# Performance work log

Measured on AMD Instinct MI355X. Metric: run time of the kernel, lower is better.

Reference implementation:

```python
import jax, jax.numpy as jnp
import numpy as np

B, T, C = 2, 2048, 2048
NH, NKV, HD = 16, 8, 256
SOFTCAP = 50.0
ROPE_BASE = 10000.0


def setup_inputs() -> dict:
    key = jax.random.key(0)
    ks = jax.random.split(key, 5)
    s = 0.02
    return {
        "X": jax.random.normal(ks[0], (B, T, C), dtype=jnp.float32),
        "Wq": jax.random.normal(ks[1], (C, NH * HD), dtype=jnp.float32) * s,
        "Wk": jax.random.normal(ks[2], (C, NKV * HD), dtype=jnp.float32) * s,
        "Wv": jax.random.normal(ks[3], (C, NKV * HD), dtype=jnp.float32) * s,
        "Wo": jax.random.normal(ks[4], (NH * HD, C), dtype=jnp.float32) * s,
    }


def _rotate_half(x):
    x1, x2 = x[..., : x.shape[-1] // 2], x[..., x.shape[-1] // 2 :]
    return jnp.concatenate((-x2, x1), axis=-1)


def _rope_cos_sin(t, head_dim, dtype):
    inv_freq = 1.0 / ROPE_BASE ** (
        jnp.arange(0, head_dim, 2, dtype=jnp.int32).astype(jnp.float32) / head_dim
    )  # [HD/2]
    pos = jnp.arange(t, dtype=jnp.float32)  # [T]
    freqs = pos[:, None] * inv_freq[None, :]  # [T, HD/2]
    emb = jnp.concatenate((freqs, freqs), axis=-1)  # [T, HD]
    # shape [1, 1, T, HD] to broadcast over (B, H, T, HD)
    return (
        jnp.cos(emb).astype(dtype)[None, None],
        jnp.sin(emb).astype(dtype)[None, None],
    )


def reference(X, Wq, Wk, Wv, Wo):
    b, t, c = X.shape
    n_rep = NH // NKV

    q = (X @ Wq).reshape(b, t, NH, HD).transpose(0, 2, 1, 3)   # [B,NH,T,HD]
    k = (X @ Wk).reshape(b, t, NKV, HD).transpose(0, 2, 1, 3)  # [B,NKV,T,HD]
    v = (X @ Wv).reshape(b, t, NKV, HD).transpose(0, 2, 1, 3)

    cos, sin = _rope_cos_sin(t, HD, X.dtype)
    q = q * cos + _rotate_half(q) * sin
    k = k * cos + _rotate_half(k) * sin

    # repeat_kv (GQA): [B,NKV,T,HD] -> [B,NH,T,HD]
    k = jnp.repeat(k, n_rep, axis=1)
    v = jnp.repeat(v, n_rep, axis=1)

    scale = 256.0 ** (-0.5)  # hardcoded in source
    att = jnp.einsum("bhqd,bhkd->bhqk", q, k) * scale
    # tanh logit softcapping
    att = SOFTCAP * jnp.tanh(att / SOFTCAP)
    # causal mask
    causal = jnp.tril(jnp.ones((t, t), dtype=bool))
    att = jnp.where(causal[None, None], att, -jnp.inf)
    att = jax.nn.softmax(att, axis=-1)

    y = jnp.einsum("bhqk,bhkd->bhqd", att, v)  # [B,NH,T,HD]
    y = y.transpose(0, 2, 1, 3).reshape(b, t, NH * HD)
    return y @ Wo
```

## Files before the change

### kernel.cpp

```cpp
#include <hip/hip_runtime.h>
#include <hip/hip_bf16.h>

#define NHD 16
#define NKVH 8
#define HDIM 256
#define TSEQ 2048
#define BATCH 2

typedef unsigned int   u32;
typedef unsigned short u16;

typedef __attribute__((ext_vector_type(8))) short bf16x8;
typedef __attribute__((ext_vector_type(4))) float floatx4;

__device__ inline u32 cvt2bf(float lo, float hi) {
  u32 r;
  asm("v_cvt_pk_bf16_f32 %0, %1, %2" : "=v"(r) : "v"(lo), "v"(hi));
  return r;
}
__device__ inline u16 f2bf(float f) {
  union { float f; u32 i; } v; v.f = f;
  u32 r = v.i + 0x7fffu + ((v.i >> 16) & 1u);
  return (u16)(r >> 16);
}
__device__ inline float bf2f(u16 u) {
  union { u32 i; float f; } v; v.i = ((u32)u) << 16; return v.f;
}
__device__ inline float fexp2(float x) {
  float r; asm("v_exp_f32 %0, %1" : "=v"(r) : "v"(x)); return r;
}
__device__ inline float fsin(float x) {
  float r; asm("v_sin_f32 %0, %1" : "=v"(r) : "v"(x)); return r;
}
__device__ inline float fcos(float x) {
  float r; asm("v_cos_f32 %0, %1" : "=v"(r) : "v"(x)); return r;
}
__device__ inline float ffract(float x) {
  float r; asm("v_fract_f32 %0, %1" : "=v"(r) : "v"(x)); return r;
}

typedef const __attribute__((address_space(1))) u32* gptr_t;
typedef __attribute__((address_space(3))) u32* lptr_t;
__device__ inline void gl_lds16(const void* g, void* l) {
  __builtin_amdgcn_global_load_lds((gptr_t)g, (lptr_t)l, 16, 0, 0);
}

__device__ inline void tconv_body(const float* __restrict__ in,
                                  u16* __restrict__ out, int R, int Cc,
                                  int bx, int by, int tid) {
  __shared__ float tile[64][65];
  const int r0 = by * 64, c0 = bx * 64;
  const int tr = tid >> 4;
  const int tc = (tid & 15) * 4;
#pragma unroll
  for (int j = 0; j < 4; ++j) {
    float4 v = *(const float4*)(in + (size_t)(r0 + tr + j * 16) * Cc + c0 + tc);
    tile[tr + j * 16][tc + 0] = v.x;
    tile[tr + j * 16][tc + 1] = v.y;
    tile[tr + j * 16][tc + 2] = v.z;
    tile[tr + j * 16][tc + 3] = v.w;
  }
  __syncthreads();
#pragma unroll
  for (int j = 0; j < 4; ++j) {
    int c = tr + j * 16;
    u16 o[4];
#pragma unroll
    for (int i = 0; i < 4; ++i) o[i] = f2bf(tile[tc + i][c]);
    *(uint2*)(out + (size_t)(c0 + c) * R + r0 + tc) = *(const uint2*)o;
  }
}

__global__ __launch_bounds__(256) void tconv_k(
    const float* __restrict__ in, u16* __restrict__ out, int R, int Cc)
{
  tconv_body(in, out, R, Cc, blockIdx.x, blockIdx.y, threadIdx.x);
}

__global__ __launch_bounds__(256) void xconv_k(
    const float* __restrict__ in, u16* __restrict__ out)
{
  size_t i = (size_t)blockIdx.x * 256 + threadIdx.x;
  float4 a = *(const float4*)(in + i * 8);
  float4 b = *(const float4*)(in + i * 8 + 4);
  uint4 o;
  o.x = cvt2bf(a.x, a.y); o.y = cvt2bf(a.z, a.w);
  o.z = cvt2bf(b.x, b.y); o.w = cvt2bf(b.z, b.w);
  *(uint4*)(out + i * 8) = o;
}

__global__ __launch_bounds__(256) void prep_k(
    const float* __restrict__ X,  const float* __restrict__ Wq,
    const float* __restrict__ Wk, const float* __restrict__ Wv,
    u16* __restrict__ XB, u16* __restrict__ WqT, u16* __restrict__ WkvT)
{
  const int bid = blockIdx.x, tid = threadIdx.x;
  if (bid < 4096) {
    size_t i = (size_t)bid * 256 + tid;
    float4 a = *(const float4*)(X + i * 8);
    float4 b = *(const float4*)(X + i * 8 + 4);
    uint4 o;
    o.x = cvt2bf(a.x, a.y); o.y = cvt2bf(a.z, a.w);
    o.z = cvt2bf(b.x, b.y); o.w = cvt2bf(b.z, b.w);
    *(uint4*)(XB + i * 8) = o;
  } else if (bid < 6144) {
    int idx = bid - 4096;
    tconv_body(Wq, WqT, 2048, 4096, idx & 63, idx >> 6, tid);
  } else if (bid < 7168) {
    int idx = bid - 6144;
    tconv_body(Wk, WkvT, 2048, 2048, idx & 31, idx >> 5, tid);
  } else {
    int idx = bid - 7168;
    tconv_body(Wv, WkvT + (size_t)2048 * 2048, 2048, 2048, idx & 31, idx >> 5, tid);
  }
}

template<int EPI, int BM>
__global__ __launch_bounds__(512, 2) void gemm256_k(
    const u16* __restrict__ Ab, const u16* __restrict__ BTp,
    void* __restrict__ Op, int M, int N, int K)
{
  constexpr int NI = BM / 32;
  constexpr int AI = BM / 64;
  __shared__ u16 LA[2][BM * 64];
  __shared__ u16 LB[2][256 * 64];
  const int t = threadIdx.x;
  const int lane = t & 63, wave = t >> 6;
  const int lg = lane >> 4, l15 = lane & 15;
  const int wm = wave >> 2, wn = wave & 3;
  const int mtiles = M / BM;
  const int mt = (int)blockIdx.x % mtiles, nt = (int)blockIdx.x / mtiles;
  const int m0 = mt * BM, n0 = nt << 8;

  const int arow = wave * (BM / 8) + (lane >> 3);
  const int ska  = ((lane & 7) ^ (arow & 7)) << 3;
  const int brow = wave * 32 + (lane >> 3);
  const int skb  = ((lane & 7) ^ (brow & 7)) << 3;
  const u16* Ag = Ab  + (size_t)(m0 + arow) * K + ska;
  const u16* Bg = BTp + (size_t)(n0 + brow) * K + skb;

  auto STAGE = [&](int k0, int sel) {
#pragma unroll
    for (int q = 0; q < AI; ++q)
      gl_lds16(Ag + k0 + (size_t)q * 8 * K, &LA[sel][(wave * (BM / 8) + q * 8) * 64]);
#pragma unroll
    for (int q = 0; q < 4; ++q)
      gl_lds16(Bg + k0 + (size_t)q * 8 * K, &LB[sel][(wave * 32 + q * 8) * 64]);
  };

  floatx4 acc[NI][4];
#pragma unroll
  for (int i = 0; i < NI; ++i)
#pragma unroll
    for (int j = 0; j < 4; ++j) acc[i][j] = (floatx4){0.f, 0.f, 0.f, 0.f};

  STAGE(0, 0);
  const int KT = K >> 6;
  for (int kt = 0; kt < KT; ++kt) {
    const int sel = kt & 1;
    if (kt + 1 < KT) {
      STAGE((kt + 1) << 6, sel ^ 1);
      if constexpr (BM == 256) asm volatile("s_waitcnt vmcnt(8)" ::: "memory");
      else                     asm volatile("s_waitcnt vmcnt(6)" ::: "memory");
    } else {
      asm volatile("s_waitcnt vmcnt(0)" ::: "memory");
    }
    __builtin_amdgcn_s_barrier();
    __builtin_amdgcn_sched_barrier(0);
    __builtin_amdgcn_s_setprio(1);
#pragma unroll
    for (int ks = 0; ks < 2; ++ks) {
      const int c = (ks << 2) + lg;
      bf16x8 bfv[4];
#pragma unroll
      for (int j = 0; j < 4; ++j) {
        int row = (EPI == 0) ? (wn * 64 + (j << 4) + l15)
                             : (wn * 32 + ((j & 1) << 4) + ((j >> 1) << 7) + l15);
        bfv[j] = *(const bf16x8*)(&LB[sel][row * 64 + ((c ^ (row & 7)) << 3)]);
      }
#pragma unroll
      for (int i = 0; i < NI; ++i) {
        int row = wm * (BM / 2) + (i << 4) + l15;
        bf16x8 af = *(const bf16x8*)(&LA[sel][row * 64 + ((c ^ (row & 7)) << 3)]);
#pragma unroll
        for (int j = 0; j < 4; ++j)
          acc[i][j] = __builtin_amdgcn_mfma_f32_16x16x32_bf16(af, bfv[j], acc[i][j], 0, 0, 0);
      }
    }
    __builtin_amdgcn_s_setprio(0);
    __builtin_amdgcn_s_barrier();
  }

  if constexpr (EPI == 0) {
#pragma unroll
    for (int i = 0; i < NI; ++i)
#pragma unroll
      for (int j = 0; j < 4; ++j)
#pragma unroll
        for (int r = 0; r < 4; ++r) {
          int m = m0 + wm * (BM / 2) + (i << 4) + (lg << 2) + r;
          int n = n0 + wn * 64 + (j << 4) + l15;
          ((float*)Op)[(size_t)m * N + n] = acc[i][j][r];
        }
  } else {
    float invf2[2];
#pragma unroll
    for (int j = 0; j < 2; ++j) {
      int col = wn * 32 + (j << 4) + l15;
      invf2[j] = fexp2(fmaf(-(float)col, 0.103810253f, -2.651496129f));
    }
#pragma unroll
    for (int i = 0; i < NI; ++i) {
#pragma unroll
      for (int j = 0; j < 2; ++j) {
        int col = wn * 32 + (j << 4) + l15;
        int n_lo = n0 + col;
#pragma unroll
        for (int r = 0; r < 4; ++r) {
          int m = m0 + wm * (BM / 2) + (i << 4) + (lg << 2) + r;
          int bb = m >> 11, tt = m & 2047;
          float vlo = acc[i][j][r], vhi = acc[i][j + 2][r];
          if (EPI == 1 || n_lo < 2048) {
            float rev = ffract((float)tt * invf2[j]);
            float sn = fsin(rev), cs = fcos(rev);
            float olo = vlo * cs - vhi * sn;
            float ohi = vhi * cs + vlo * sn;
            vlo = olo; vhi = ohi;
          }
          if (EPI == 1) {
            int h = n_lo >> 8;
            u16* dst = (u16*)Op + (((size_t)bb * NHD + h) * TSEQ + tt) * HDIM + col;
            dst[0]   = f2bf(vlo);
            dst[128] = f2bf(vhi);
          } else {
            if (n_lo < 2048) {
              int h = n_lo >> 8;
              u16* dst = (u16*)Op + (((size_t)bb * NKVH + h) * TSEQ + tt) * HDIM + col;
              dst[0]   = f2bf(vlo);
              dst[128] = f2bf(vhi);
            } else {
              int n2 = n_lo - 2048;
              int h = n2 >> 8;
              u16* dst = (u16*)Op + 8388608u +
                         (((size_t)bb * NKVH + h) * HDIM + col) * TSEQ + tt;
              dst[0] = f2bf(vlo);
              dst[(size_t)128 * TSEQ] = f2bf(vhi);
            }
          }
        }
      }
    }
  }
}

__global__ __launch_bounds__(512, 2) void attn_k(
    const u16* __restrict__ Q, const u16* __restrict__ Kb,
    const u16* __restrict__ Vt, u16* __restrict__ Y)
{
  __shared__ u16 Ks2[2][32 * 256];
  __shared__ u16 Vs[256 * 32];
  __shared__ u16 Ps[8 * 16 * 32];
  __shared__ float Ls[8][16];
  const int t = threadIdx.x, lane = t & 63, w = t >> 6;
  const int lg = lane >> 4, l15 = lane & 15;
  const int hq = w >> 2, wq = w & 3;
  const int qt = 31 - (int)blockIdx.y;
  const int hkv = (int)blockIdx.x >> 1, b = (int)blockIdx.x & 1;
  const int h = 2 * hkv + hq;

  const u16* Kg = Kb + ((size_t)(b * NKVH + hkv)) * TSEQ * HDIM;
  const u16* Vg = Vt + ((size_t)(b * NKVH + hkv)) * HDIM * TSEQ;

  int koff[2], voff[2];
#pragma unroll
  for (int q = 0; q < 2; ++q) {
    int krow = w * 4 + q * 2 + (lane >> 5);
    int kcc  = lane & 31;
    koff[q] = krow * 256 + ((kcc ^ (krow & 7)) << 3);
    int vd  = w * 32 + q * 16 + (lane >> 2);
    voff[q] = vd * TSEQ + (((lane & 3) ^ ((vd >> 2) & 3)) << 3);
  }

  auto STAGE_K = [&](int st, int sel) {
    const u16* kbase = Kg + (size_t)st * (32 * 256);
#pragma unroll
    for (int q = 0; q < 2; ++q)
      gl_lds16(kbase + koff[q], &Ks2[sel][(w * 4 + q * 2) * 256]);
  };
  auto STAGE_V = [&](int st) {
    const u16* vbase = Vg + st * 32;
#pragma unroll
    for (int q = 0; q < 2; ++q)
      gl_lds16(vbase + voff[q], &Vs[(w * 32 + q * 16) * 32]);
  };

  const u16* Qg = Q + (((size_t)(b * NHD + h)) * TSEQ + qt * 64 + wq * 16 + l15) * HDIM;
  bf16x8 qf[8];
#pragma unroll
  for (int ks = 0; ks < 8; ++ks) qf[ks] = *(const bf16x8*)(Qg + ks * 32 + lg * 8);

  floatx4 accY[16];
#pragma unroll
  for (int i = 0; i < 16; ++i) accY[i] = (floatx4){0.f, 0.f, 0.f, 0.f};
  float rsum = 0.f;

  const int qglob = qt * 64 + wq * 16 + l15;
  const int qmaxw = qt * 64 + wq * 16 + 15;
  const int nst = 2 * qt + 2;
  const int fps = (l15 ^ (l15 >> 2)) & 3;

  STAGE_K(0, 0);
  for (int st = 0; st < nst; ++st) {
    const int sel = st & 1;
    STAGE_V(st);
    if (st + 1 < nst) {
      STAGE_K(st + 1, sel ^ 1);
      asm volatile("s_waitcnt vmcnt(4)" ::: "memory");
    } else {
      asm volatile("s_waitcnt vmcnt(2)" ::: "memory");
    }
    __builtin_amdgcn_s_barrier();
    __builtin_amdgcn_sched_barrier(0);

    if (st * 32 <= qmaxw) {
      __builtin_amdgcn_s_setprio(1);
#pragma unroll
      for (int stile = 0; stile < 2; ++stile) {
        floatx4 sa0 = (floatx4){0.f, 0.f, 0.f, 0.f};
        floatx4 sa1 = (floatx4){0.f, 0.f, 0.f, 0.f};
#pragma unroll
        for (int ks = 0; ks < 8; ++ks) {
          int row = (stile << 4) + l15;
          int c = (ks << 2) + lg;
          bf16x8 kf = *(const bf16x8*)((const char*)Ks2[sel] +
                        row * 512 + ((c ^ (row & 7)) << 4));
          if (ks & 1)
            sa1 = __builtin_amdgcn_mfma_f32_16x16x32_bf16(kf, qf[ks], sa1, 0, 0, 0);
          else
            sa0 = __builtin_amdgcn_mfma_f32_16x16x32_bf16(kf, qf[ks], sa0, 0, 0, 0);
        }
        int sbase = st * 32 + (stile << 4) + (lg << 2);
        float p[4];
#pragma unroll
        for (int r = 0; r < 4; ++r) {
          float s = sa0[r] + sa1[r];
          float tt = fmaf(s * s, -5.2083333e-7f, 1.0f);
          float pv = fexp2(s * 0.0901684403f * tt);
          pv = (sbase + r <= qglob) ? pv : 0.0f;
          p[r] = pv;
          rsum += pv;
        }
        uint2 pw;
        pw.x = cvt2bf(p[0], p[1]);
        pw.y = cvt2bf(p[2], p[3]);
        int o = (stile << 5) + (lg << 3);
        int gran = (o >> 4) ^ fps;
        *(uint2*)((char*)Ps + (w << 10) + l15 * 64 + (gran << 4) + (o & 15)) = pw;
      }
      __builtin_amdgcn_s_setprio(0);
    }

    if (st + 1 < nst)
      asm volatile("s_waitcnt vmcnt(2)" ::: "memory");
    else
      asm volatile("s_waitcnt vmcnt(0)" ::: "memory");
    __builtin_amdgcn_s_barrier();
    __builtin_amdgcn_sched_barrier(0);

    if (st * 32 <= qmaxw) {
      __builtin_amdgcn_s_setprio(1);
      bf16x8 pf = *(const bf16x8*)((const char*)Ps + (w << 10) + l15 * 64 +
                    ((lg ^ fps) << 4));
#pragma unroll
      for (int dt = 0; dt < 16; ++dt) {
        int row = (dt << 4) + l15;
        bf16x8 vf = *(const bf16x8*)((const char*)Vs +
                      row * 64 + ((lg ^ ((row >> 2) & 3)) << 4));
        accY[dt] = __builtin_amdgcn_mfma_f32_16x16x32_bf16(pf, vf, accY[dt], 0, 0, 0);
      }
      __builtin_amdgcn_s_setprio(0);
    }
    __builtin_amdgcn_s_barrier();
  }

  rsum += __shfl_xor(rsum, 16);
  rsum += __shfl_xor(rsum, 32);
  if (lane < 16) Ls[w][l15] = rsum;
  __syncthreads();
  float inv[4];
#pragma unroll
  for (int r = 0; r < 4; ++r) inv[r] = 1.0f / Ls[w][(lg << 2) + r];

  u16* Yg = Y + ((size_t)(b * TSEQ + qt * 64 + wq * 16)) * (NHD * HDIM) + h * HDIM;
#pragma unroll
  for (int dt = 0; dt < 16; ++dt)
#pragma unroll
    for (int r = 0; r < 4; ++r)
      Yg[(size_t)((lg << 2) + r) * (NHD * HDIM) + (dt << 4) + l15] =
          f2bf(accY[dt][r] * inv[r]);
}

extern "C" void kernel_launch(void* const* d_in, const int* in_sizes, int n_in,
                              void* d_out, int out_size, void* d_ws, size_t ws_size,
                              hipStream_t stream) {
  const float* X  = (const float*)d_in[0];
  const float* Wq = (const float*)d_in[1];
  const float* Wk = (const float*)d_in[2];
  const float* Wv = (const float*)d_in[3];
  const float* Wo = (const float*)d_in[4];
  float* out = (float*)d_out;

  u16* ws = (u16*)d_ws;
  dim3 blk(256);

  if (ws_size >= (size_t)117440512) {
    u16* XB   = ws;
    u16* WqT  = ws + 8388608;
    u16* WkvT = ws + 16777216;
    u16* Qb   = ws + 25165824;
    u16* KVb  = ws + 41943040;
    u16* Yb   = ws;
    u16* WoT  = ws + 25165824;

    prep_k<<<dim3(8192), blk, 0, stream>>>(X, Wq, Wk, Wv, XB, WqT, WkvT);
    gemm256_k<1, 256><<<dim3(256), dim3(512), 0, stream>>>(XB, WqT,  Qb,  4096, 4096, 2048);
    gemm256_k<3, 256><<<dim3(256), dim3(512), 0, stream>>>(XB, WkvT, KVb, 4096, 4096, 2048);
    attn_k<<<dim3(16, 32), dim3(512), 0, stream>>>(Qb, KVb, KVb + 8388608, Yb);
    tconv_k<<<dim3(32, 64), blk, 0, stream>>>(Wo, WoT, 4096, 2048);
    gemm256_k<0, 128><<<dim3(256), dim3(512), 0, stream>>>(Yb, WoT, out, 4096, 2048, 4096);
  } else {
    u16* XB   = ws;
    u16* WT   = ws + 8388608;
    u16* Qb   = ws + 16777216;
    u16* KVb  = ws + 33554432;
    u16* Yb   = ws;
    u16* WoT  = ws + 16777216;

    xconv_k<<<dim3(4096), blk, 0, stream>>>(X, XB);
    tconv_k<<<dim3(64, 32), blk, 0, stream>>>(Wq, WT, 2048, 4096);
    gemm256_k<1, 256><<<dim3(256), dim3(512), 0, stream>>>(XB, WT, Qb, 4096, 4096, 2048);
    tconv_k<<<dim3(32, 32), blk, 0, stream>>>(Wk, WT, 2048, 2048);
    tconv_k<<<dim3(32, 32), blk, 0, stream>>>(Wv, WT + (size_t)2048 * 2048, 2048, 2048);
    gemm256_k<3, 256><<<dim3(256), dim3(512), 0, stream>>>(XB, WT, KVb, 4096, 4096, 2048);
    attn_k<<<dim3(16, 32), dim3(512), 0, stream>>>(Qb, KVb, KVb + 8388608, Yb);
    tconv_k<<<dim3(32, 64), blk, 0, stream>>>(Wo, WoT, 4096, 2048);
    gemm256_k<0, 128><<<dim3(256), dim3(512), 0, stream>>>(Yb, WoT, out, 4096, 2048, 4096);
  }
}
```

Before: 395.3 us.

## Double-buffer V tiles in attention and fold Wo transpose into prep kernel

The attention kernel now double-buffers the V tile alongside K, so both are prefetched one stage ahead. This removes the second wait-and-barrier that used to sit between the score computation and the P·V MFMAs in every iteration. Separately, when the workspace is large enough, the Wo transpose/convert is merged into the prep kernel, dropping a separate launch. The cost is more LDS per block for the second V buffer, which may affect occupancy. The new path also requires a larger workspace to be active.

New measurement: 409.2 us. +3.5%, slower.

```diff
diff --git a/kernel.cpp b/kernel.cpp
--- a/kernel.cpp
+++ b/kernel.cpp
@@ -92,7 +92,9 @@
 __global__ __launch_bounds__(256) void prep_k(
     const float* __restrict__ X,  const float* __restrict__ Wq,
     const float* __restrict__ Wk, const float* __restrict__ Wv,
-    u16* __restrict__ XB, u16* __restrict__ WqT, u16* __restrict__ WkvT)
+    const float* __restrict__ Wo,
+    u16* __restrict__ XB, u16* __restrict__ WqT, u16* __restrict__ WkvT,
+    u16* __restrict__ WoT)
 {
   const int bid = blockIdx.x, tid = threadIdx.x;
   if (bid < 4096) {
@@ -109,9 +111,12 @@
   } else if (bid < 7168) {
     int idx = bid - 6144;
     tconv_body(Wk, WkvT, 2048, 2048, idx & 31, idx >> 5, tid);
-  } else {
+  } else if (bid < 8192) {
     int idx = bid - 7168;
     tconv_body(Wv, WkvT + (size_t)2048 * 2048, 2048, 2048, idx & 31, idx >> 5, tid);
+  } else {
+    int idx = bid - 8192;
+    tconv_body(Wo, WoT, 4096, 2048, idx & 31, idx >> 5, tid);
   }
 }
 
@@ -258,7 +263,7 @@
     const u16* __restrict__ Vt, u16* __restrict__ Y)
 {
   __shared__ u16 Ks2[2][32 * 256];
-  __shared__ u16 Vs[256 * 32];
+  __shared__ u16 Vs2[2][256 * 32];
   __shared__ u16 Ps[8 * 16 * 32];
   __shared__ float Ls[8][16];
   const int t = threadIdx.x, lane = t & 63, w = t >> 6;
@@ -281,17 +286,15 @@
     voff[q] = vd * TSEQ + (((lane & 3) ^ ((vd >> 2) & 3)) << 3);
   }
 
-  auto STAGE_K = [&](int st, int sel) {
+  auto STAGE = [&](int st, int sel) {
     const u16* kbase = Kg + (size_t)st * (32 * 256);
+    const u16* vbase = Vg + st * 32;
 #pragma unroll
     for (int q = 0; q < 2; ++q)
       gl_lds16(kbase + koff[q], &Ks2[sel][(w * 4 + q * 2) * 256]);
-  };
-  auto STAGE_V = [&](int st) {
-    const u16* vbase = Vg + st * 32;
 #pragma unroll
     for (int q = 0; q < 2; ++q)
-      gl_lds16(vbase + voff[q], &Vs[(w * 32 + q * 16) * 32]);
+      gl_lds16(vbase + voff[q], &Vs2[sel][(w * 32 + q * 16) * 32]);
   };
 
   const u16* Qg = Q + (((size_t)(b * NHD + h)) * TSEQ + qt * 64 + wq * 16 + l15) * HDIM;
@@ -309,15 +312,14 @@
   const int nst = 2 * qt + 2;
   const int fps = (l15 ^ (l15 >> 2)) & 3;
 
-  STAGE_K(0, 0);
+  STAGE(0, 0);
   for (int st = 0; st < nst; ++st) {
     const int sel = st & 1;
-    STAGE_V(st);
     if (st + 1 < nst) {
-      STAGE_K(st + 1, sel ^ 1);
+      STAGE(st + 1, sel ^ 1);
       asm volatile("s_waitcnt vmcnt(4)" ::: "memory");
     } else {
-      asm volatile("s_waitcnt vmcnt(2)" ::: "memory");
+      asm volatile("s_waitcnt vmcnt(0)" ::: "memory");
     }
     __builtin_amdgcn_s_barrier();
     __builtin_amdgcn_sched_barrier(0);
@@ -357,26 +359,16 @@
         int gran = (o >> 4) ^ fps;
         *(uint2*)((char*)Ps + (w << 10) + l15 * 64 + (gran << 4) + (o & 15)) = pw;
       }
-      __builtin_amdgcn_s_setprio(0);
-    }
-
-    if (st + 1 < nst)
-      asm volatile("s_waitcnt vmcnt(2)" ::: "memory");
-    else
-      asm volatile("s_waitcnt vmcnt(0)" ::: "memory");
-    __builtin_amdgcn_s_barrier();
-    __builtin_amdgcn_sched_barrier(0);
-
-    if (st * 32 <= qmaxw) {
-      __builtin_amdgcn_s_setprio(1);
-      bf16x8 pf = *(const bf16x8*)((const char*)Ps + (w << 10) + l15 * 64 +
-                    ((lg ^ fps) << 4));
-#pragma unroll
-      for (int dt = 0; dt < 16; ++dt) {
-        int row = (dt << 4) + l15;
-        bf16x8 vf = *(const bf16x8*)((const char*)Vs +
-                      row * 64 + ((lg ^ ((row >> 2) & 3)) << 4));
-        accY[dt] = __builtin_amdgcn_mfma_f32_16x16x32_bf16(pf, vf, accY[dt], 0, 0, 0);
+      {
+        bf16x8 pf = *(const bf16x8*)((const char*)Ps + (w << 10) + l15 * 64 +
+                      ((lg ^ fps) << 4));
+#pragma unroll
+        for (int dt = 0; dt < 16; ++dt) {
+          int row = (dt << 4) + l15;
+          bf16x8 vf = *(const bf16x8*)((const char*)Vs2[sel] +
+                        row * 64 + ((lg ^ ((row >> 2) & 3)) << 4));
+          accY[dt] = __builtin_amdgcn_mfma_f32_16x16x32_bf16(pf, vf, accY[dt], 0, 0, 0);
+        }
       }
       __builtin_amdgcn_s_setprio(0);
     }
@@ -413,7 +405,21 @@
   u16* ws = (u16*)d_ws;
   dim3 blk(256);
 
-  if (ws_size >= (size_t)117440512) {
+  if (ws_size >= (size_t)134217728) {
+    u16* XB   = ws;
+    u16* WqT  = ws + 8388608;
+    u16* WkvT = ws + 16777216;
+    u16* Qb   = ws + 25165824;
+    u16* KVb  = ws + 41943040;
+    u16* WoT  = ws + 58720256;
+    u16* Yb   = ws;
+
+    prep_k<<<dim3(10240), blk, 0, stream>>>(X, Wq, Wk, Wv, Wo, XB, WqT, WkvT, WoT);
+    gemm256_k<1, 256><<<dim3(256), dim3(512), 0, stream>>>(XB, WqT,  Qb,  4096, 4096, 2048);
+    gemm256_k<3, 256><<<dim3(256), dim3(512), 0, stream>>>(XB, WkvT, KVb, 4096, 4096, 2048);
+    attn_k<<<dim3(16, 32), dim3(512), 0, stream>>>(Qb, KVb, KVb + 8388608, Yb);
+    gemm256_k<0, 128><<<dim3(256), dim3(512), 0, stream>>>(Yb, WoT, out, 4096, 2048, 4096);
+  } else if (ws_size >= (size_t)117440512) {
     u16* XB   = ws;
     u16* WqT  = ws + 8388608;
     u16* WkvT = ws + 16777216;
@@ -422,7 +428,7 @@
     u16* Yb   = ws;
     u16* WoT  = ws + 25165824;
 
-    prep_k<<<dim3(8192), blk, 0, stream>>>(X, Wq, Wk, Wv, XB, WqT, WkvT);
+    prep_k<<<dim3(8192), blk, 0, stream>>>(X, Wq, Wk, Wv, Wo, XB, WqT, WkvT, WkvT);
     gemm256_k<1, 256><<<dim3(256), dim3(512), 0, stream>>>(XB, WqT,  Qb,  4096, 4096, 2048);
     gemm256_k<3, 256><<<dim3(256), dim3(512), 0, stream>>>(XB, WkvT, KVb, 4096, 4096, 2048);
     attn_k<<<dim3(16, 32), dim3(512), 0, stream>>>(Qb, KVb, KVb + 8388608, Yb);
```
